# Kernel optimization log

Hardware: AMD Instinct MI355X
Metric: run time of the kernel (lower is better)

## Reference

```python
import jax, jax.numpy as jnp
import numpy as np

N = 50000          # nodes
E = 800000         # edges (before self-loops)
IN_DIM = 128
HID = 64           # hidden_dim (per-head out channels)
HEADS = 2
NL = 3             # num_layers of GATConv
CH = HEADS * HID   # 128, per-layer node feature width
LSTM_H = (2 * CH) // 2  # 128, PyG JumpingKnowledge lstm hidden size (num_layers=2)
NEG_SLOPE = 0.2


def setup_inputs() -> dict:
    key = jax.random.key(0)
    ks = jax.random.split(key, 24)
    r = lambda i, shape, s=0.1: jax.random.normal(ks[i], shape, dtype=jnp.float32) * s
    return {
        "x": jax.random.normal(ks[0], (N, IN_DIM), dtype=jnp.float32),
        "edge_index": jax.random.randint(ks[1], (2, E), 0, N),
        "W1": r(2, (CH, IN_DIM)),
        "att1_src": r(3, (HEADS, HID)),
        "att1_dst": r(4, (HEADS, HID)),
        "b1": r(5, (CH,)),
        "Ws": r(6, (NL - 1, CH, CH)),
        "atts_src": r(7, (NL - 1, HEADS, HID)),
        "atts_dst": r(8, (NL - 1, HEADS, HID)),
        "bs": r(9, (NL - 1, CH)),
        "lstm_Wih": r(10, (2, 4 * LSTM_H, CH)),
        "lstm_Whh": r(11, (2, 4 * LSTM_H, LSTM_H)),
        "lstm_bih": r(12, (2, 4 * LSTM_H)),
        "lstm_bhh": r(13, (2, 4 * LSTM_H)),
        "jk_att_w": r(14, (1, 2 * LSTM_H)),
        "jk_att_b": r(15, (1,)),
        "lin1_w": r(16, (HID, CH)),
        "lin1_b": r(17, (HID,)),
        "lin2_w": r(18, (HID, HID + IN_DIM)),
        "lin2_b": r(19, (HID,)),
        "out_w": r(20, (6, HID)),
        "out_b": r(21, (6,)),
    }


def _gat(x, src, dst, W, a_src, a_dst, b):
    # PyG GATConv: linear -> per-head attention logits -> segment softmax over
    # incoming edges -> weighted scatter-add -> concat heads + bias.
    xp = (x @ W.T).reshape(N, HEADS, HID)          # [N,H,C]
    es = jnp.sum(xp * a_src, -1)                   # [N,H]
    ed = jnp.sum(xp * a_dst, -1)                   # [N,H]
    e = jax.nn.leaky_relu(es[src] + ed[dst], NEG_SLOPE)  # [E,H]
    m = jax.ops.segment_max(e, dst, num_segments=N)
    ex = jnp.exp(e - m[dst])
    s = jax.ops.segment_sum(ex, dst, num_segments=N)
    alpha = ex / s[dst]                            # [E,H]
    out = jax.ops.segment_sum(xp[src] * alpha[..., None], dst, num_segments=N)
    return out.reshape(N, CH) + b


def _lstm_dir(seq, Wih, Whh, bih, bhh, reverse):
    # seq: [L, N, CH]; torch gate order (i, f, g, o)
    def step(carry, xt):
        h, c = carry
        g = xt @ Wih.T + bih + h @ Whh.T + bhh
        i, f, gg, o = jnp.split(g, 4, axis=-1)
        c = jax.nn.sigmoid(f) * c + jax.nn.sigmoid(i) * jnp.tanh(gg)
        h = jax.nn.sigmoid(o) * jnp.tanh(c)
        return (h, c), h
    z = jnp.zeros((seq.shape[1], LSTM_H), seq.dtype)
    _, hs = jax.lax.scan(step, (z, z), seq, reverse=reverse)
    return hs  # [L, N, LSTM_H]


def reference(x, edge_index, W1, att1_src, att1_dst, b1, Ws, atts_src, atts_dst, bs,
              lstm_Wih, lstm_Whh, lstm_bih, lstm_bhh, jk_att_w, jk_att_b,
              lin1_w, lin1_b, lin2_w, lin2_b, out_w, out_b):
    loops = jnp.arange(N)
    src = jnp.concatenate([edge_index[0], loops])  # PyG adds self-loops
    dst = jnp.concatenate([edge_index[1], loops])

    h = _gat(x, src, dst, W1, att1_src, att1_dst, b1)  # conv1: no relu on xs[0]
    xs = [h]
    for l in range(NL - 1):
        h = jax.nn.relu(_gat(h, src, dst, Ws[l], atts_src[l], atts_dst[l], bs[l]))
        xs.append(h)

    # JumpingKnowledge 'lstm': biLSTM over layer axis, attention-weighted sum.
    X = jnp.stack(xs, axis=0)                       # [L, N, CH]
    hf = _lstm_dir(X, lstm_Wih[0], lstm_Whh[0], lstm_bih[0], lstm_bhh[0], False)
    hb = _lstm_dir(X, lstm_Wih[1], lstm_Whh[1], lstm_bih[1], lstm_bhh[1], True)
    hcat = jnp.concatenate([hf, hb], -1)            # [L, N, 2*LSTM_H]
    score = (hcat @ jk_att_w.T + jk_att_b)[..., 0]  # [L, N]
    alpha = jax.nn.softmax(score, axis=0)
    jk = jnp.sum(X * alpha[..., None], axis=0)      # [N, CH]

    h1 = jax.nn.relu(jk @ lin1_w.T + lin1_b)        # dropout is identity (eval)
    h2 = jax.nn.relu(jnp.concatenate([h1, x], axis=1) @ lin2_w.T + lin2_b)
    logits = h2 @ out_w.T + out_b
    return jax.nn.log_softmax(logits, axis=1)
```

## Files before the change

kernel.cpp:

```cpp
#include <hip/hip_runtime.h>
#include <math.h>

#define CDIV(a,b) (((a)+(b)-1)/(b))

typedef __attribute__((ext_vector_type(8))) short bfrag;
typedef __attribute__((ext_vector_type(4))) float ffrag;

__device__ inline unsigned short f2bf(float f) {
    unsigned int u = __float_as_uint(f);
    return (unsigned short)((u + 0x7fffu + ((u >> 16) & 1u)) >> 16);
}
__device__ inline float bf2f(unsigned short u) {
    return __uint_as_float(((unsigned int)u) << 16);
}
__device__ inline float sigf(float x) {
    return __builtin_amdgcn_rcpf(1.f + __expf(-x));
}
__device__ inline float tanhfast(float x) {
    float t = __expf(-2.f * fabsf(x));
    float r = (1.f - t) * __builtin_amdgcn_rcpf(1.f + t);
    return copysignf(r, x);
}
__device__ inline int hoff(int row, int k) {
    int sw = ((k >> 3) ^ row) & 15;
    return row * 128 + sw * 8 + (k & 7);
}

__global__ void zero_i32(int* __restrict__ p, int n) {
    int i = blockIdx.x * 256 + threadIdx.x;
    if (i < n) p[i] = 0;
}
__global__ void init_score_k(float* __restrict__ sc, const float* __restrict__ b, int n) {
    int i = blockIdx.x * 256 + threadIdx.x;
    if (i < n) sc[i] = b[0];
}

__global__ void prep_k(const float* __restrict__ Wih, const float* __restrict__ Whh,
                       const float* __restrict__ bih, const float* __restrict__ bhh,
                       unsigned short* __restrict__ Wp, float* __restrict__ bsum,
                       const float* __restrict__ W1, const float* __restrict__ Ws,
                       const float* __restrict__ l1w, const float* __restrict__ l2w,
                       unsigned short* __restrict__ wb,
                       const float* __restrict__ x, unsigned short* __restrict__ xb, int nx) {
    int i = blockIdx.x * 256 + threadIdx.x;
    if (i < 1024) bsum[i] = bih[i] + bhh[i];
    if (i < 262144) {
        int k = i & 255, j = (i >> 8) & 511, d = i >> 17;
        float v = (k < 128) ? Wih[((size_t)d * 512 + j) * 128 + k]
                            : Whh[((size_t)d * 512 + j) * 128 + (k - 128)];
        Wp[i] = f2bf(v);
        return;
    }
    int i2 = i - 262144;
    if (i2 < 69632) {
        float v;
        if (i2 < 16384)      v = W1[i2];
        else if (i2 < 49152) v = Ws[i2 - 16384];
        else if (i2 < 57344) v = l1w[i2 - 49152];
        else                 v = l2w[i2 - 57344];
        wb[i2] = f2bf(v);
        return;
    }
    int i3 = i2 - 69632;
    if (i3 < nx) xb[i3] = f2bf(x[i3]);
}

__global__ void hist_k(const int* __restrict__ ei, int E, int ET, int* __restrict__ deg) {
    int e = blockIdx.x * 256 + threadIdx.x;
    if (e >= ET) return;
    int d = (e < E) ? ei[E + e] : e - E;
    atomicAdd(deg + d, 1);
}

__global__ __launch_bounds__(256)
void scan1_k(const int* __restrict__ deg, int* __restrict__ row_ptr,
             int* __restrict__ part, int Nn) {
    __shared__ int ls[256];
    int t = threadIdx.x;
    int base = blockIdx.x * 1024 + t * 4;
    int v[4];
    #pragma unroll
    for (int j = 0; j < 4; ++j) v[j] = (base + j < Nn) ? deg[base + j] : 0;
    int s = v[0] + v[1] + v[2] + v[3];
    ls[t] = s;
    __syncthreads();
    for (int off = 1; off < 256; off <<= 1) {
        int o = (t >= off) ? ls[t - off] : 0;
        __syncthreads();
        ls[t] += o;
        __syncthreads();
    }
    int run = ls[t] - s;
    if (t == 255) part[blockIdx.x] = ls[255];
    #pragma unroll
    for (int j = 0; j < 4; ++j) {
        if (base + j < Nn) row_ptr[base + j] = run;
        run += v[j];
    }
}
__global__ void scan2_k(int* __restrict__ part, int nb) {
    int lane = threadIdx.x;
    int v = (lane < nb) ? part[lane] : 0;
    int orig = v;
    for (int off = 1; off < 64; off <<= 1) {
        int o = __shfl_up(v, off);
        if (lane >= off) v += o;
    }
    if (lane < nb) part[lane] = v - orig;
}
__global__ void scan3_k(const int* __restrict__ part, int* __restrict__ row_ptr,
                        int* __restrict__ cursor, int Nn) {
    int i = blockIdx.x * 256 + threadIdx.x;
    if (i >= Nn) return;
    int v = row_ptr[i] + part[i >> 10];
    row_ptr[i] = v;
    cursor[i] = v;
}

__global__ void fill_k(const int* __restrict__ ei, int E, int ET,
                       int* __restrict__ cursor, int* __restrict__ csr_src) {
    int e = blockIdx.x * 256 + threadIdx.x;
    if (e >= ET) return;
    int s, d;
    if (e < E) { s = ei[e]; d = ei[E + e]; } else { s = e - E; d = s; }
    int pos = atomicAdd(cursor + d, 1);
    csr_src[pos] = s;
}

template<int NT, int K, int K1, bool RELU, bool FUSE, bool BFOUT>
__global__ __launch_bounds__(256)
void gemm_mfma_k(const unsigned short* __restrict__ A1, const unsigned short* __restrict__ A2,
                 int ldA2, const unsigned short* __restrict__ Wb, const float* __restrict__ bias,
                 unsigned short* __restrict__ Cb, float* __restrict__ Cf,
                 const float* __restrict__ asl, const float* __restrict__ adl,
                 float* __restrict__ es, float* __restrict__ ed, int M)
{
    int tid = threadIdx.x;
    int wv = tid >> 6, lane = tid & 63;
    int col = lane & 15, kg = lane >> 4;
    int row0 = blockIdx.x * 64 + wv * 16;
    int mrow = row0 + col;
    bool mok = mrow < M;

    ffrag acc[NT];
    #pragma unroll
    for (int t = 0; t < NT; ++t) acc[t] = (ffrag){0.f, 0.f, 0.f, 0.f};

    #pragma unroll
    for (int ks = 0; ks < K / 32; ++ks) {
        int kk = ks * 32 + kg * 8;
        bfrag a = (bfrag){0,0,0,0,0,0,0,0};
        if (mok) {
            if (kk < K1) a = *(const bfrag*)(A1 + (size_t)mrow * K1 + kk);
            else         a = *(const bfrag*)(A2 + (size_t)mrow * ldA2 + (kk - K1));
        }
        #pragma unroll
        for (int t = 0; t < NT; ++t) {
            bfrag b = *(const bfrag*)(Wb + (size_t)(t * 16 + col) * K + kk);
            acc[t] = __builtin_amdgcn_mfma_f32_16x16x32_bf16(a, b, acc[t], 0, 0, 0);
        }
    }

    #pragma unroll
    for (int r = 0; r < 4; ++r) {
        int n = row0 + kg * 4 + r;
        bool ok = n < M;
        float e0 = 0.f, e1 = 0.f, d0 = 0.f, d1 = 0.f;
        #pragma unroll
        for (int t = 0; t < NT; ++t) {
            float v = acc[t][r];
            if (FUSE) {
                int ch = t * 16 + col;
                if (t < NT / 2) { e0 = fmaf(v, asl[ch], e0); d0 = fmaf(v, adl[ch], d0); }
                else            { e1 = fmaf(v, asl[ch], e1); d1 = fmaf(v, adl[ch], d1); }
            }
            if (bias) v += bias[t * 16 + col];
            if (RELU) v = fmaxf(v, 0.f);
            if (ok) {
                if (BFOUT) Cb[(size_t)n * (NT * 16) + t * 16 + col] = f2bf(v);
                else       Cf[(size_t)n * (NT * 16) + t * 16 + col] = v;
            }
        }
        if (FUSE) {
            #pragma unroll
            for (int mk = 1; mk < 16; mk <<= 1) {
                e0 += __shfl_xor(e0, mk); e1 += __shfl_xor(e1, mk);
                d0 += __shfl_xor(d0, mk); d1 += __shfl_xor(d1, mk);
            }
            if (col == 0 && ok) {
                es[n * 2] = e0; es[n * 2 + 1] = e1;
                ed[n * 2] = d0; ed[n * 2 + 1] = d1;
            }
        }
    }
}

__global__ __launch_bounds__(256)
void gat_agg_k(const int* __restrict__ csr_src, const int* __restrict__ row_ptr,
               const int* __restrict__ deg,
               const unsigned short* __restrict__ xpb, const float* __restrict__ es,
               const float* __restrict__ ed, const float* __restrict__ bias,
               unsigned short* __restrict__ out, int Nn, int relu)
{
    int wid = (blockIdx.x * 256 + threadIdx.x) >> 6;
    int lane = threadIdx.x & 63;
    if (wid >= Nn) return;
    int n = wid;
    int beg = row_ptr[n];
    int dn = deg[n];
    float2 edv = *(const float2*)(ed + n * 2);

    int   src_c = 0;
    float z0_c = 0.f, z1_c = 0.f;
    float m0 = -3e38f, m1 = -3e38f, s0 = 0.f, s1 = 0.f;
    for (int i = lane; i < dn; i += 64) {
        int s = csr_src[beg + i];
        float2 e2 = *(const float2*)(es + s * 2);
        float z0 = e2.x + edv.x; z0 = z0 > 0.f ? z0 : 0.2f * z0;
        float z1 = e2.y + edv.y; z1 = z1 > 0.f ? z1 : 0.2f * z1;
        if (i == lane) { src_c = s; z0_c = z0; z1_c = z1; }
        float nm0 = fmaxf(m0, z0);
        s0 = s0 * __expf(m0 - nm0) + __expf(z0 - nm0); m0 = nm0;
        float nm1 = fmaxf(m1, z1);
        s1 = s1 * __expf(m1 - nm1) + __expf(z1 - nm1); m1 = nm1;
    }
    #pragma unroll
    for (int off = 32; off; off >>= 1) {
        float om0 = __shfl_xor(m0, off), os0 = __shfl_xor(s0, off);
        float nm0 = fmaxf(m0, om0);
        s0 = s0 * __expf(m0 - nm0) + os0 * __expf(om0 - nm0); m0 = nm0;
        float om1 = __shfl_xor(m1, off), os1 = __shfl_xor(s1, off);
        float nm1 = fmaxf(m1, om1);
        s1 = s1 * __expf(m1 - nm1) + os1 * __expf(om1 - nm1); m1 = nm1;
    }
    float inv0 = 1.f / s0, inv1 = 1.f / s1;

    float acc0 = 0.f, acc1 = 0.f;
    if (dn <= 64) {
        float a0_c = __expf(z0_c - m0) * inv0;
        float a1_c = __expf(z1_c - m1) * inv1;
        #pragma unroll 8
        for (int i = 0; i < dn; ++i) {
            int s = __shfl(src_c, i);
            float a0 = __shfl(a0_c, i);
            float a1 = __shfl(a1_c, i);
            float aw = (lane < 32) ? a0 : a1;
            unsigned int u = *(const unsigned int*)(xpb + (size_t)s * 128 + 2 * lane);
            acc0 = fmaf(bf2f((unsigned short)(u & 0xffff)), aw, acc0);
            acc1 = fmaf(bf2f((unsigned short)(u >> 16)), aw, acc1);
        }
    } else {
        for (int i = 0; i < dn; ++i) {
            int s = csr_src[beg + i];
            float2 e2 = *(const float2*)(es + s * 2);
            float z0 = e2.x + edv.x; z0 = z0 > 0.f ? z0 : 0.2f * z0;
            float z1 = e2.y + edv.y; z1 = z1 > 0.f ? z1 : 0.2f * z1;
            float a0 = __expf(z0 - m0) * inv0;
            float a1 = __expf(z1 - m1) * inv1;
            float aw = (lane < 32) ? a0 : a1;
            unsigned int u = *(const unsigned int*)(xpb + (size_t)s * 128 + 2 * lane);
            acc0 = fmaf(bf2f((unsigned short)(u & 0xffff)), aw, acc0);
            acc1 = fmaf(bf2f((unsigned short)(u >> 16)), aw, acc1);
        }
    }
    float2 bb = *(const float2*)(bias + 2 * lane);
    float v0 = acc0 + bb.x;
    float v1 = acc1 + bb.y;
    if (relu) { v0 = fmaxf(v0, 0.f); v1 = fmaxf(v1, 0.f); }
    unsigned int o = (unsigned int)f2bf(v0) | ((unsigned int)f2bf(v1) << 16);
    *(unsigned int*)(out + (size_t)n * 128 + 2 * lane) = o;
}

__global__ __launch_bounds__(512)
void lstm_all_k(const unsigned short* __restrict__ X0, const unsigned short* __restrict__ X1,
                const unsigned short* __restrict__ X2,
                const unsigned short* __restrict__ WpB, const float* __restrict__ bsumB,
                const float* __restrict__ jkw, float* __restrict__ score, int Nn, int ntiles)
{
    __shared__ unsigned short h_lds[2][32 * 128];
    int dir = blockIdx.y;
    const unsigned short* Xs0 = dir ? X2 : X0;
    const unsigned short* Xs2 = dir ? X0 : X2;
    const unsigned short* Wp = WpB + (size_t)dir * 512 * 256;
    const float* bsum = bsumB + dir * 512;
    const float* wsc = jkw + dir * 128;

    int tid = threadIdx.x;
    int wv = tid >> 6, lane = tid & 63;
    int col = lane & 15, kg = lane >> 4;
    int t0 = dir ? 2 : 0;
    int kch = 16 * wv + col;
    float bi = bsum[kch], bf_ = bsum[128 + kch];
    float bg = bsum[256 + kch], bo = bsum[384 + kch];
    float wk = wsc[kch];

    bfrag wreg[4][8];
    #pragma unroll
    for (int g = 0; g < 4; ++g) {
        const unsigned short* wrow = Wp + (size_t)(16 * (8 * g + wv) + col) * 256;
        #pragma unroll
        for (int ks = 0; ks < 8; ++ks)
            wreg[g][ks] = *(const bfrag*)(wrow + ks * 32 + kg * 8);
    }

    for (int tile = blockIdx.x; tile < ntiles; tile += gridDim.x) {
        int node0 = tile * 32;
        float c[2][4] = {};

        #pragma unroll
        for (int i = 0; i < 3; ++i) {
            int t = (i == 0) ? t0 : ((i == 1) ? 1 : (2 - t0));
            const unsigned short* Xt = (i == 0) ? Xs0 : ((i == 1) ? X1 : Xs2);
            const unsigned short* h_rd = h_lds[(i + 1) & 1];
            unsigned short* h_wr = h_lds[i & 1];

            ffrag acc[2][4];
            #pragma unroll
            for (int nt = 0; nt < 2; ++nt)
                #pragma unroll
                for (int g = 0; g < 4; ++g) acc[nt][g] = (ffrag){0.f, 0.f, 0.f, 0.f};

            #pragma unroll
            for (int ks = 0; ks < 4; ++ks) {
                int kk = ks * 32 + kg * 8;
                bfrag a0 = *(const bfrag*)(Xt + (size_t)(node0 + col) * 128 + kk);
                bfrag a1 = *(const bfrag*)(Xt + (size_t)(node0 + 16 + col) * 128 + kk);
                #pragma unroll
                for (int g = 0; g < 4; ++g) {
                    acc[0][g] = __builtin_amdgcn_mfma_f32_16x16x32_bf16(a0, wreg[g][ks], acc[0][g], 0, 0, 0);
                    acc[1][g] = __builtin_amdgcn_mfma_f32_16x16x32_bf16(a1, wreg[g][ks], acc[1][g], 0, 0, 0);
                }
            }

            if (i > 0) {
                #pragma unroll
                for (int ks = 4; ks < 8; ++ks) {
                    int kh = (ks - 4) * 32 + kg * 8;
                    bfrag ah0 = *(const bfrag*)&h_rd[hoff(col, kh)];
                    bfrag ah1 = *(const bfrag*)&h_rd[hoff(16 + col, kh)];
                    #pragma unroll
                    for (int g = 0; g < 4; ++g) {
                        acc[0][g] = __builtin_amdgcn_mfma_f32_16x16x32_bf16(ah0, wreg[g][ks], acc[0][g], 0, 0, 0);
                        acc[1][g] = __builtin_amdgcn_mfma_f32_16x16x32_bf16(ah1, wreg[g][ks], acc[1][g], 0, 0, 0);
                    }
                }
            }

            #pragma unroll
            for (int nt = 0; nt < 2; ++nt) {
                #pragma unroll
                for (int r = 0; r < 4; ++r) {
                    float gi = acc[nt][0][r] + bi;
                    float gf = acc[nt][1][r] + bf_;
                    float gg = acc[nt][2][r] + bg;
                    float go = acc[nt][3][r] + bo;
                    float si = sigf(gi);
                    float sf = sigf(gf);
                    float so = sigf(go);
                    float tg = tanhfast(gg);
                    float cn = sf * c[nt][r] + si * tg;
                    float hn = so * tanhfast(cn);
                    c[nt][r] = cn;
                    int nl = nt * 16 + kg * 4 + r;
                    h_wr[hoff(nl, kch)] = f2bf(hn);
                    float v = hn * wk;
                    #pragma unroll
                    for (int mk = 1; mk < 16; mk <<= 1) v += __shfl_xor(v, mk);
                    if (col == 0) {
                        int n = node0 + nl;
                        if (n < Nn) atomicAdd(&score[(size_t)t * Nn + n], v);
                    }
                }
            }
            __syncthreads();
        }
    }
}

__global__ void jk_combine_k(const float* __restrict__ score, const unsigned short* __restrict__ x0,
                             const unsigned short* __restrict__ x1, const unsigned short* __restrict__ x2,
                             unsigned short* __restrict__ jkb, int N_) {
    int gid = blockIdx.x * 256 + threadIdx.x;
    int n = gid >> 5;
    if (n >= N_) return;
    int c = (gid & 31) * 4;
    float s0 = score[n], s1 = score[N_ + n], s2 = score[2*N_ + n];
    float mx = fmaxf(s0, fmaxf(s1, s2));
    float e0 = __expf(s0 - mx), e1 = __expf(s1 - mx), e2 = __expf(s2 - mx);
    float inv = 1.f / (e0 + e1 + e2);
    float a0 = e0 * inv, a1 = e1 * inv, a2 = e2 * inv;
    size_t off = (size_t)n * 128 + c;
    ushort4 u0 = *(const ushort4*)(x0 + off);
    ushort4 u1 = *(const ushort4*)(x1 + off);
    ushort4 u2 = *(const ushort4*)(x2 + off);
    ushort4 o;
    o.x = f2bf(a0*bf2f(u0.x) + a1*bf2f(u1.x) + a2*bf2f(u2.x));
    o.y = f2bf(a0*bf2f(u0.y) + a1*bf2f(u1.y) + a2*bf2f(u2.y));
    o.z = f2bf(a0*bf2f(u0.z) + a1*bf2f(u1.z) + a2*bf2f(u2.z));
    o.w = f2bf(a0*bf2f(u0.w) + a1*bf2f(u1.w) + a2*bf2f(u2.w));
    *(ushort4*)(jkb + off) = o;
}

__global__ void final_out_k(const float* __restrict__ h2, const float* __restrict__ ow,
                            const float* __restrict__ ob, float* __restrict__ out, int N_) {
    int n = blockIdx.x * 256 + threadIdx.x;
    if (n >= N_) return;
    float l[6];
    #pragma unroll
    for (int j = 0; j < 6; ++j) l[j] = ob[j];
    for (int c = 0; c < 64; c += 4) {
        float4 h4 = *(const float4*)(h2 + (size_t)n * 64 + c);
        #pragma unroll
        for (int j = 0; j < 6; ++j) {
            l[j] += h4.x * ow[j*64 + c + 0] + h4.y * ow[j*64 + c + 1]
                  + h4.z * ow[j*64 + c + 2] + h4.w * ow[j*64 + c + 3];
        }
    }
    float mx = l[0];
    #pragma unroll
    for (int j = 1; j < 6; ++j) mx = fmaxf(mx, l[j]);
    float se = 0.f;
    #pragma unroll
    for (int j = 0; j < 6; ++j) se += __expf(l[j] - mx);
    float ls = logf(se) + mx;
    #pragma unroll
    for (int j = 0; j < 6; ++j) out[(size_t)n * 6 + j] = l[j] - ls;
}

extern "C" void kernel_launch(void* const* d_in, const int* in_sizes, int n_in,
                              void* d_out, int out_size, void* d_ws, size_t ws_size,
                              hipStream_t stream) {
    const float* x   = (const float*)d_in[0];
    const int*   ei  = (const int*)d_in[1];
    const float* W1  = (const float*)d_in[2];
    const float* a1s = (const float*)d_in[3];
    const float* a1d = (const float*)d_in[4];
    const float* b1  = (const float*)d_in[5];
    const float* Ws  = (const float*)d_in[6];
    const float* ass = (const float*)d_in[7];
    const float* asd = (const float*)d_in[8];
    const float* bs  = (const float*)d_in[9];
    const float* Wih = (const float*)d_in[10];
    const float* Whh = (const float*)d_in[11];
    const float* bih = (const float*)d_in[12];
    const float* bhh = (const float*)d_in[13];
    const float* jkw = (const float*)d_in[14];
    const float* jkb_b = (const float*)d_in[15];
    const float* l1w = (const float*)d_in[16];
    const float* l1b = (const float*)d_in[17];
    const float* l2w = (const float*)d_in[18];
    const float* l2b = (const float*)d_in[19];
    const float* ow  = (const float*)d_in[20];
    const float* ob  = (const float*)d_in[21];
    float* out = (float*)d_out;

    int Nn = in_sizes[0] / 128;
    int E  = in_sizes[1] / 2;
    int ET = E + Nn;
    size_t Np = ((size_t)Nn + 63) & ~(size_t)63;
    size_t Fp = Np * 128;

    float* w = (float*)d_ws;
    float* es    = w;
    float* ed    = es + 2*Nn;
    float* score = ed + 2*Nn;
    float* bsum  = score + 3*Nn;
    float* h2    = bsum + 1024;
    unsigned short* xb   = (unsigned short*)(h2 + (size_t)Nn*64);
    unsigned short* xpb  = xb + Fp;
    unsigned short* xsb0 = xpb + Fp;
    unsigned short* xsb1 = xsb0 + Fp;
    unsigned short* xsb2 = xsb1 + Fp;
    unsigned short* h1b  = xsb2 + Fp;
    unsigned short* Wp   = h1b + Fp;
    unsigned short* wb   = Wp + 2*512*256;
    int* deg     = (int*)(wb + 69632);
    int* row_ptr = deg + Nn;
    int* cursor  = row_ptr + Nn;
    int* part    = cursor + Nn;
    int* csr_src = part + 64;
    unsigned short* jkb = xpb;

    int nb1 = CDIV(Nn, 1024);
    zero_i32<<<CDIV(Nn, 256), 256, 0, stream>>>(deg, Nn);
    hist_k<<<CDIV(ET, 256), 256, 0, stream>>>(ei, E, ET, deg);
    scan1_k<<<nb1, 256, 0, stream>>>(deg, row_ptr, part, Nn);
    scan2_k<<<1, 64, 0, stream>>>(part, nb1);
    scan3_k<<<CDIV(Nn, 256), 256, 0, stream>>>(part, row_ptr, cursor, Nn);
    fill_k<<<CDIV(ET, 256), 256, 0, stream>>>(ei, E, ET, cursor, csr_src);

    int nprep = 262144 + 69632 + Nn * 128;
    prep_k<<<CDIV(nprep, 256), 256, 0, stream>>>(Wih, Whh, bih, bhh, Wp, bsum,
                                                 W1, Ws, l1w, l2w, wb, x, xb, Nn * 128);

    unsigned short* xsb_arr[3] = {xsb0, xsb1, xsb2};
    int gblk = CDIV(Nn, 64);

    for (int l = 0; l < 3; ++l) {
        const float* asl = (l == 0) ? a1s : ass + (size_t)(l-1) * 128;
        const float* adl = (l == 0) ? a1d : asd + (size_t)(l-1) * 128;
        const float* bl  = (l == 0) ? b1  : bs  + (size_t)(l-1) * 128;
        const unsigned short* Ain = (l == 0) ? xb : xsb_arr[l-1];
        const unsigned short* Wbl = wb + (size_t)l * 16384;
        gemm_mfma_k<8,128,128,false,true,true><<<gblk, 256, 0, stream>>>(
            Ain, Ain, 128, Wbl, nullptr, xpb, nullptr, asl, adl, es, ed, Nn);
        gat_agg_k<<<CDIV(Nn, 4), 256, 0, stream>>>(csr_src, row_ptr, deg, xpb, es, ed, bl,
                                                   xsb_arr[l], Nn, l > 0);
    }

    init_score_k<<<CDIV(3*Nn, 256), 256, 0, stream>>>(score, jkb_b, 3*Nn);
    int ntiles = CDIV(Nn, 32);
    int gx = ntiles < 256 ? ntiles : 256;
    lstm_all_k<<<dim3(gx, 2), 512, 0, stream>>>(xsb0, xsb1, xsb2, Wp, bsum, jkw, score, Nn, ntiles);

    jk_combine_k<<<CDIV(Nn*32, 256), 256, 0, stream>>>(score, xsb0, xsb1, xsb2, jkb, Nn);
    gemm_mfma_k<4,128,128,true,false,true><<<gblk, 256, 0, stream>>>(
        jkb, jkb, 128, wb + 49152, l1b, h1b, nullptr, nullptr, nullptr, nullptr, nullptr, Nn);
    gemm_mfma_k<4,192,64,true,false,false><<<gblk, 256, 0, stream>>>(
        h1b, xb, 128, wb + 57344, l2b, nullptr, h2, nullptr, nullptr, nullptr, nullptr, Nn);
    final_out_k<<<CDIV(Nn, 256), 256, 0, stream>>>(h2, ow, ob, out, Nn);
}
```

Before: 627.6 us.

## Accumulate LSTM attention scores in shared memory, drop init kernel and global atomics

The LSTM kernel now accumulates each tile's per-node attention score contributions with shared-memory atomics and writes them with plain stores into a separate buffer per direction. This removes the global atomicAdd traffic and the score initialisation kernel. The combine kernel adds the bias and sums the two direction buffers itself. The LSTM grid width is also halved from 256 to 128 blocks per direction, which reduces parallelism, and each tile gains two extra block barriers.

```diff
diff --git a/kernel.cpp b/kernel.cpp
--- a/kernel.cpp
+++ b/kernel.cpp
@@ -29,10 +29,6 @@
 __global__ void zero_i32(int* __restrict__ p, int n) {
     int i = blockIdx.x * 256 + threadIdx.x;
     if (i < n) p[i] = 0;
-}
-__global__ void init_score_k(float* __restrict__ sc, const float* __restrict__ b, int n) {
-    int i = blockIdx.x * 256 + threadIdx.x;
-    if (i < n) sc[i] = b[0];
 }
 
 __global__ void prep_k(const float* __restrict__ Wih, const float* __restrict__ Whh,
@@ -278,12 +274,14 @@
                 const float* __restrict__ jkw, float* __restrict__ score, int Nn, int ntiles)
 {
     __shared__ unsigned short h_lds[2][32 * 128];
+    __shared__ float sc_s[96];
     int dir = blockIdx.y;
     const unsigned short* Xs0 = dir ? X2 : X0;
     const unsigned short* Xs2 = dir ? X0 : X2;
     const unsigned short* Wp = WpB + (size_t)dir * 512 * 256;
     const float* bsum = bsumB + dir * 512;
     const float* wsc = jkw + dir * 128;
+    float* scD = score + (size_t)dir * 3 * Nn;
 
     int tid = threadIdx.x;
     int wv = tid >> 6, lane = tid & 63;
@@ -306,10 +304,11 @@
     for (int tile = blockIdx.x; tile < ntiles; tile += gridDim.x) {
         int node0 = tile * 32;
         float c[2][4] = {};
+        if (tid < 96) sc_s[tid] = 0.f;
+        __syncthreads();
 
         #pragma unroll
         for (int i = 0; i < 3; ++i) {
-            int t = (i == 0) ? t0 : ((i == 1) ? 1 : (2 - t0));
             const unsigned short* Xt = (i == 0) ? Xs0 : ((i == 1) ? X1 : Xs2);
             const unsigned short* h_rd = h_lds[(i + 1) & 1];
             unsigned short* h_wr = h_lds[i & 1];
@@ -366,25 +365,35 @@
                     float v = hn * wk;
                     #pragma unroll
                     for (int mk = 1; mk < 16; mk <<= 1) v += __shfl_xor(v, mk);
-                    if (col == 0) {
-                        int n = node0 + nl;
-                        if (n < Nn) atomicAdd(&score[(size_t)t * Nn + n], v);
-                    }
+                    if (col == 0) atomicAdd(&sc_s[i * 32 + nl], v);
                 }
             }
             __syncthreads();
         }
-    }
-}
-
-__global__ void jk_combine_k(const float* __restrict__ score, const unsigned short* __restrict__ x0,
+
+        if (tid < 96) {
+            int ii = tid >> 5, nl = tid & 31;
+            int t = (ii == 0) ? t0 : ((ii == 1) ? 1 : (2 - t0));
+            int n = node0 + nl;
+            if (n < Nn) scD[(size_t)t * Nn + n] = sc_s[tid];
+        }
+        __syncthreads();
+    }
+}
+
+__global__ void jk_combine_k(const float* __restrict__ scA, const float* __restrict__ scB,
+                             const float* __restrict__ jkbias,
+                             const unsigned short* __restrict__ x0,
                              const unsigned short* __restrict__ x1, const unsigned short* __restrict__ x2,
                              unsigned short* __restrict__ jkb, int N_) {
     int gid = blockIdx.x * 256 + threadIdx.x;
     int n = gid >> 5;
     if (n >= N_) return;
     int c = (gid & 31) * 4;
-    float s0 = score[n], s1 = score[N_ + n], s2 = score[2*N_ + n];
+    float b = jkbias[0];
+    float s0 = b + scA[n] + scB[n];
+    float s1 = b + scA[N_ + n] + scB[N_ + n];
+    float s2 = b + scA[2*N_ + n] + scB[2*N_ + n];
     float mx = fmaxf(s0, fmaxf(s1, s2));
     float e0 = __expf(s0 - mx), e1 = __expf(s1 - mx), e2 = __expf(s2 - mx);
     float inv = 1.f / (e0 + e1 + e2);
@@ -464,7 +473,7 @@
     float* es    = w;
     float* ed    = es + 2*Nn;
     float* score = ed + 2*Nn;
-    float* bsum  = score + 3*Nn;
+    float* bsum  = score + 6*Nn;
     float* h2    = bsum + 1024;
     unsigned short* xb   = (unsigned short*)(h2 + (size_t)Nn*64);
     unsigned short* xpb  = xb + Fp;
@@ -508,12 +517,12 @@
                                                    xsb_arr[l], Nn, l > 0);
     }
 
-    init_score_k<<<CDIV(3*Nn, 256), 256, 0, stream>>>(score, jkb_b, 3*Nn);
     int ntiles = CDIV(Nn, 32);
-    int gx = ntiles < 256 ? ntiles : 256;
+    int gx = ntiles < 128 ? ntiles : 128;
     lstm_all_k<<<dim3(gx, 2), 512, 0, stream>>>(xsb0, xsb1, xsb2, Wp, bsum, jkw, score, Nn, ntiles);
 
-    jk_combine_k<<<CDIV(Nn*32, 256), 256, 0, stream>>>(score, xsb0, xsb1, xsb2, jkb, Nn);
+    jk_combine_k<<<CDIV(Nn*32, 256), 256, 0, stream>>>(score, score + (size_t)3*Nn, jkb_b,
+                                                       xsb0, xsb1, xsb2, jkb, Nn);
     gemm_mfma_k<4,128,128,true,false,true><<<gblk, 256, 0, stream>>>(
         jkb, jkb, 128, wb + 49152, l1b, h1b, nullptr, nullptr, nullptr, nullptr, nullptr, Nn);
     gemm_mfma_k<4,192,64,true,false,false><<<gblk, 256, 0, stream>>>(
```

New measurement: 605.1 us. 1.04x faster.
